# Performance work log

Hardware: AMD Instinct MI355X
Metric: run time of the kernel (lower is better)

Reference implementation:

```python
import jax, jax.numpy as jnp
import numpy as np

B, T, C, H = 8, 1024, 768, 12
M = 8  # extra rows in feats left as zeros (n = M + B*T)
N = M + B * T


def setup_inputs() -> dict:
    key = jax.random.key(0)
    k1, k2, k3, k4, k5 = jax.random.split(key, 5)
    feats = jax.random.normal(k1, (N, C), dtype=jnp.float32)
    amask = jax.random.randint(k2, (B, T), 0, 2).astype(bool)
    Wqkv = jax.random.normal(k3, (3 * C, C), dtype=jnp.float32) * 0.02
    Wp = jax.random.normal(k4, (C, C), dtype=jnp.float32) * 0.02
    bp = jax.random.normal(k5, (C,), dtype=jnp.float32) * 0.001
    return {"feats": feats, "amask": amask, "Wqkv": Wqkv, "Wp": Wp, "bp": bp}


def reference(feats, amask, Wqkv, Wp, bp):
    b, t = amask.shape
    n, c = feats.shape
    m = n - b * t          # rows of feats not touched by attention (stay zero)
    h = H
    d = c // h
    scale = d ** -0.5
    mf = amask.reshape(-1)                      # [b*t] bool
    x = feats[m:]                               # [b*t, c]

    # MaskedLinear(qkv): gather->GEMM->scatter == dense GEMM zeroed at masked-out rows
    qkv = jnp.where(mf[:, None], x @ Wqkv.T, jnp.zeros((), x.dtype))  # [b*t, 3c]
    qkv = qkv.reshape(b, t, 3, h, d).transpose(2, 0, 3, 1, 4)          # [3,b,h,t,d]
    q, k, v = qkv[0], qkv[1], qkv[2]

    # dense SDPA (no attn mask, matching F.scaled_dot_product_attention default)
    att = jax.nn.softmax(jnp.einsum('bhqd,bhkd->bhqk', q, k) * scale, axis=-1)
    o = jnp.einsum('bhqk,bhkd->bhqd', att, v)                          # [b,h,t,d]
    o = o.transpose(0, 2, 1, 3).reshape(b * t, c)                      # [b*t, c]

    # MaskedLinear(proj) with bias; masked-out rows are zero (not bias)
    o = jnp.where(mf[:, None], o @ Wp.T + bp, jnp.zeros((), o.dtype))

    # scatter back into a zero tensor of feats' shape (first m rows zero)
    return jnp.concatenate([jnp.zeros((m, c), feats.dtype), o], axis=0)
```

## Files before the change

### kernel.cpp

```cpp
#include <hip/hip_runtime.h>
#include <hip/hip_bf16.h>


#define BB 8
#define TT 1024
#define CC 768
#define HH 12
#define DD 64
#define MM 8
#define NTOK (BB*TT)
#define NX (NTOK*CC)
#define NWQ (3*CC*CC)
#define NWP (CC*CC)
#define QSCALE 0.18033688011112042f

typedef short bf16x8 __attribute__((ext_vector_type(8)));
typedef float f32x4  __attribute__((ext_vector_type(4)));
typedef float f32x16 __attribute__((ext_vector_type(16)));

__device__ __forceinline__ void gld16(const void* g, void* l) {
  __builtin_amdgcn_global_load_lds(
      (const __attribute__((address_space(1))) void*)g,
      (__attribute__((address_space(3))) void*)l, 16, 0, 0);
}

__device__ __forceinline__ short bf_rne(float f) {
  unsigned u = __float_as_uint(f);
  return (short)((u + 0x7FFFu + ((u >> 16) & 1u)) >> 16);
}
__device__ __forceinline__ short bf_split(float f, short& lo) {
  unsigned u = __float_as_uint(f);
  unsigned hb = (u + 0x7FFFu + ((u >> 16) & 1u)) >> 16;
  float r = f - __uint_as_float(hb << 16);
  lo = bf_rne(r);
  return (short)hb;
}

__global__ __launch_bounds__(256) void split_inputs(
    const float* __restrict__ x, const float* __restrict__ wq,
    const float* __restrict__ wp,
    short* __restrict__ xh, short* __restrict__ wqh,
    short* __restrict__ wph, short* __restrict__ wpl) {
  const int G0 = NX/4, G1 = G0 + NWQ/4, G2 = G1 + NWP/4;
  int i = blockIdx.x * 256 + threadIdx.x;
  if (i >= G2) return;
  if (i < G1) {
    const float* src = (i < G0) ? x : wq;
    short* dh = (i < G0) ? xh : wqh;
    int li = (i < G0) ? i : i - G0;
    float4 v = *(const float4*)(src + (size_t)li * 4);
    short4 h;
    h.x = bf_rne(v.x); h.y = bf_rne(v.y); h.z = bf_rne(v.z); h.w = bf_rne(v.w);
    *(short4*)(dh + (size_t)li * 4) = h;
  } else {
    int li = i - G1;
    float4 v = *(const float4*)(wp + (size_t)li * 4);
    short4 h, l;
    h.x = bf_split(v.x, l.x);
    h.y = bf_split(v.y, l.y);
    h.z = bf_split(v.z, l.z);
    h.w = bf_split(v.w, l.w);
    *(short4*)(wph + (size_t)li * 4) = h;
    *(short4*)(wpl + (size_t)li * 4) = l;
  }
}

template<bool TRIPLE>
__device__ __forceinline__ void gemm_core_768(
    const short* __restrict__ ah_g, const short* __restrict__ al_g,
    const short* __restrict__ bh_g, const short* __restrict__ bl_g,
    int m0, int n0, f32x16 (&acc)[2][2],
    int& wm_o, int& wn_o) {
  __shared__ __align__(16) short Ah[128*32], Bh[128*32];
  __shared__ __align__(16) short Al[TRIPLE ? 128*32 : 16];
  __shared__ __align__(16) short Bl[TRIPLE ? 128*32 : 16];
  const int tid = threadIdx.x;
  const int w = tid >> 6, ln = tid & 63;
  const int wm = (w >> 1) * 64, wn = (w & 1) * 64;
  const int sr = ln >> 2, sc = (ln & 3) * 8;
  const int l31 = ln & 31, lhi = ln >> 5;
  const int c0 = 2*w, c1 = 2*w + 1;
  const short* gAh0 = ah_g + (size_t)(m0 + c0*16 + sr)*CC + sc;
  const short* gAh1 = ah_g + (size_t)(m0 + c1*16 + sr)*CC + sc;
  const short* gBh0 = bh_g + (size_t)(n0 + c0*16 + sr)*CC + sc;
  const short* gBh1 = bh_g + (size_t)(n0 + c1*16 + sr)*CC + sc;
  const short* gAl0 = TRIPLE ? al_g + (size_t)(m0 + c0*16 + sr)*CC + sc : nullptr;
  const short* gAl1 = TRIPLE ? al_g + (size_t)(m0 + c1*16 + sr)*CC + sc : nullptr;
  const short* gBl0 = TRIPLE ? bl_g + (size_t)(n0 + c0*16 + sr)*CC + sc : nullptr;
  const short* gBl1 = TRIPLE ? bl_g + (size_t)(n0 + c1*16 + sr)*CC + sc : nullptr;
  #pragma unroll
  for (int i = 0; i < 2; i++)
    #pragma unroll
    for (int j = 0; j < 2; j++)
      #pragma unroll
      for (int r = 0; r < 16; r++) acc[i][j][r] = 0.f;

  for (int it = 0; it < 24; ++it) {
    const int ko = it * 32;
    gld16(gAh0 + ko, &Ah[c0*512]);
    gld16(gAh1 + ko, &Ah[c1*512]);
    gld16(gBh0 + ko, &Bh[c0*512]);
    gld16(gBh1 + ko, &Bh[c1*512]);
    if constexpr (TRIPLE) {
      gld16(gAl0 + ko, &Al[c0*512]);
      gld16(gAl1 + ko, &Al[c1*512]);
      gld16(gBl0 + ko, &Bl[c0*512]);
      gld16(gBl1 + ko, &Bl[c1*512]);
    }
    __syncthreads();
    bf16x8 a_h[2][2], b_h[2][2];
    #pragma unroll
    for (int t = 0; t < 2; ++t)
      #pragma unroll
      for (int kc = 0; kc < 2; ++kc) {
        a_h[t][kc] = *(const bf16x8*)&Ah[(wm + t*32 + l31)*32 + kc*16 + lhi*8];
        b_h[t][kc] = *(const bf16x8*)&Bh[(wn + t*32 + l31)*32 + kc*16 + lhi*8];
      }
    if constexpr (TRIPLE) {
      bf16x8 a_l[2][2], b_l[2][2];
      #pragma unroll
      for (int t = 0; t < 2; ++t)
        #pragma unroll
        for (int kc = 0; kc < 2; ++kc) {
          a_l[t][kc] = *(const bf16x8*)&Al[(wm + t*32 + l31)*32 + kc*16 + lhi*8];
          b_l[t][kc] = *(const bf16x8*)&Bl[(wn + t*32 + l31)*32 + kc*16 + lhi*8];
        }
      #pragma unroll
      for (int mt = 0; mt < 2; ++mt)
        #pragma unroll
        for (int nt = 0; nt < 2; ++nt)
          #pragma unroll
          for (int kc = 0; kc < 2; ++kc) {
            acc[mt][nt] = __builtin_amdgcn_mfma_f32_32x32x16_bf16(
                a_h[mt][kc], b_h[nt][kc], acc[mt][nt], 0, 0, 0);
            acc[mt][nt] = __builtin_amdgcn_mfma_f32_32x32x16_bf16(
                a_h[mt][kc], b_l[nt][kc], acc[mt][nt], 0, 0, 0);
            acc[mt][nt] = __builtin_amdgcn_mfma_f32_32x32x16_bf16(
                a_l[mt][kc], b_h[nt][kc], acc[mt][nt], 0, 0, 0);
          }
    } else {
      #pragma unroll
      for (int mt = 0; mt < 2; ++mt)
        #pragma unroll
        for (int nt = 0; nt < 2; ++nt)
          #pragma unroll
          for (int kc = 0; kc < 2; ++kc)
            acc[mt][nt] = __builtin_amdgcn_mfma_f32_32x32x16_bf16(
                a_h[mt][kc], b_h[nt][kc], acc[mt][nt], 0, 0, 0);
    }
    __syncthreads();
  }
  wm_o = wm; wn_o = wn;
}

__global__ __launch_bounds__(256) void qkv_mfma(
    const short* __restrict__ ah_g, const short* __restrict__ bh_g,
    const int* __restrict__ mask,
    short* __restrict__ qb, short* __restrict__ kb, short* __restrict__ vb) {
  const int m0 = blockIdx.y * 128, n0 = blockIdx.x * 128;
  f32x16 acc[2][2];
  int wm, wn;
  gemm_core_768<false>(ah_g, nullptr, bh_g, nullptr, m0, n0, acc, wm, wn);
  const int ln = threadIdx.x & 63;
  const int l31 = ln & 31, lhi = ln >> 5;
  const int s = n0 / CC;
  short* dst = (s == 0) ? qb : ((s == 1) ? kb : vb);
  const float qs = (s == 0) ? QSCALE : 1.f;
  const int nb = n0 % CC;
  #pragma unroll
  for (int mt = 0; mt < 2; ++mt) {
    #pragma unroll
    for (int reg = 0; reg < 16; ++reg) {
      int row = m0 + wm + mt*32 + 4*lhi + (reg & 3) + 8*(reg >> 2);
      int mk = mask[row];
      int b = row >> 10, t = row & 1023;
      size_t rb = ((size_t)b * HH) * TT;
      #pragma unroll
      for (int nt = 0; nt < 2; ++nt) {
        int gnb = nb + wn + nt*32 + l31;
        int h = gnb >> 6, d = gnb & 63;
        float v = mk ? acc[mt][nt][reg] * qs : 0.f;
        dst[((rb + (size_t)h * TT) + t) * DD + d] = bf_rne(v);
      }
    }
  }
}

__global__ __launch_bounds__(256) void proj_mfma(
    const short* __restrict__ ah_g, const short* __restrict__ al_g,
    const short* __restrict__ bh_g, const short* __restrict__ bl_g,
    const int* __restrict__ mask, const float* __restrict__ bp,
    float* __restrict__ out) {
  const int m0 = blockIdx.y * 128, n0 = blockIdx.x * 128;
  f32x16 acc[2][2];
  int wm, wn;
  gemm_core_768<true>(ah_g, al_g, bh_g, bl_g, m0, n0, acc, wm, wn);
  const int ln = threadIdx.x & 63;
  const int l31 = ln & 31, lhi = ln >> 5;
  #pragma unroll
  for (int mt = 0; mt < 2; ++mt) {
    #pragma unroll
    for (int reg = 0; reg < 16; ++reg) {
      int row = m0 + wm + mt*32 + 4*lhi + (reg & 3) + 8*(reg >> 2);
      int mk = mask[row];
      float* orow = out + (size_t)(MM + row) * CC;
      #pragma unroll
      for (int nt = 0; nt < 2; ++nt) {
        int gn = n0 + wn + nt*32 + l31;
        orow[gn] = mk ? acc[mt][nt][reg] + bp[gn] : 0.f;
      }
    }
  }
}

__global__ __launch_bounds__(256) void attn_mfma(
    const short* __restrict__ qb, const short* __restrict__ kb,
    const short* __restrict__ vb, const int* __restrict__ mask,
    short* __restrict__ obh, short* __restrict__ obl) {
  __shared__ __align__(16) short Ks[64][72];
  __shared__ __align__(16) short Vt[64][72];
  __shared__ __align__(16) short Ps[4][32][72];
  const int tid = threadIdx.x, w = tid >> 6, ln = tid & 63;
  const int fl = ln & 15, fq = ln >> 4;
  const int bh = blockIdx.x >> 3;
  const int q0 = (blockIdx.x & 7) * 128;
  const int b = bh / HH, h = bh % HH;
  const size_t base = (size_t)bh * TT * DD;

  bf16x8 qf[2][2];
  #pragma unroll
  for (int mt = 0; mt < 2; ++mt)
    #pragma unroll
    for (int kc = 0; kc < 2; ++kc)
      qf[mt][kc] = *(const bf16x8*)&qb[base +
          (size_t)(q0 + w*32 + mt*16 + fl) * DD + kc*32 + fq*8];

  f32x4 oa[2][4];
  float lsum[2][4];
  {
    f32x4 z = {0.f, 0.f, 0.f, 0.f};
    #pragma unroll
    for (int mt = 0; mt < 2; ++mt) {
      #pragma unroll
      for (int nt = 0; nt < 4; ++nt) oa[mt][nt] = z;
      #pragma unroll
      for (int r = 0; r < 4; ++r) lsum[mt][r] = 0.f;
    }
  }

  const int skey = tid >> 2, sch = (tid & 3) * 2;
  const int vkey = tid & 63, vd0 = (tid >> 6) * 16;

  for (int kt = 0; kt < 16; ++kt) {
    __syncthreads();
    {
      const short* kg = &kb[base + (size_t)(kt*64 + skey) * DD + sch*8];
      bf16x8 k0 = *(const bf16x8*)kg;
      bf16x8 k1 = *(const bf16x8*)(kg + 8);
      *(bf16x8*)&Ks[skey][sch*8] = k0;
      *(bf16x8*)&Ks[skey][sch*8 + 8] = k1;
      const short* vg = &vb[base + (size_t)(kt*64 + vkey) * DD + vd0];
      bf16x8 v0 = *(const bf16x8*)vg;
      bf16x8 v1 = *(const bf16x8*)(vg + 8);
      #pragma unroll
      for (int j = 0; j < 8; ++j) {
        Vt[vd0 + j][vkey] = v0[j];
        Vt[vd0 + 8 + j][vkey] = v1[j];
      }
    }
    __syncthreads();

    bf16x8 kf[4][2], vf[4][2];
    #pragma unroll
    for (int nt = 0; nt < 4; ++nt)
      #pragma unroll
      for (int kc = 0; kc < 2; ++kc) {
        kf[nt][kc] = *(const bf16x8*)&Ks[nt*16 + fl][kc*32 + fq*8];
        vf[nt][kc] = *(const bf16x8*)&Vt[nt*16 + fl][kc*32 + fq*8];
      }

    f32x4 s[2][4];
    {
      f32x4 z = {0.f, 0.f, 0.f, 0.f};
      #pragma unroll
      for (int mt = 0; mt < 2; ++mt)
        #pragma unroll
        for (int nt = 0; nt < 4; ++nt) s[mt][nt] = z;
    }
    #pragma unroll
    for (int mt = 0; mt < 2; ++mt)
      #pragma unroll
      for (int nt = 0; nt < 4; ++nt) {
        s[mt][nt] = __builtin_amdgcn_mfma_f32_16x16x32_bf16(
            qf[mt][0], kf[nt][0], s[mt][nt], 0, 0, 0);
        s[mt][nt] = __builtin_amdgcn_mfma_f32_16x16x32_bf16(
            qf[mt][1], kf[nt][1], s[mt][nt], 0, 0, 0);
      }

    #pragma unroll
    for (int mt = 0; mt < 2; ++mt)
      #pragma unroll
      for (int nt = 0; nt < 4; ++nt)
        #pragma unroll
        for (int r = 0; r < 4; ++r) {
          float p = __builtin_amdgcn_exp2f(s[mt][nt][r]);
          unsigned pu = __float_as_uint(p);
          lsum[mt][r] += __uint_as_float(pu & 0xFFFF0000u);
          Ps[w][mt*16 + fq*4 + r][nt*16 + fl] = (short)(pu >> 16);
        }

    bf16x8 pf[2][2];
    #pragma unroll
    for (int mt = 0; mt < 2; ++mt)
      #pragma unroll
      for (int kc = 0; kc < 2; ++kc)
        pf[mt][kc] = *(const bf16x8*)&Ps[w][mt*16 + fl][kc*32 + fq*8];

    #pragma unroll
    for (int mt = 0; mt < 2; ++mt)
      #pragma unroll
      for (int nt = 0; nt < 4; ++nt) {
        oa[mt][nt] = __builtin_amdgcn_mfma_f32_16x16x32_bf16(
            pf[mt][0], vf[nt][0], oa[mt][nt], 0, 0, 0);
        oa[mt][nt] = __builtin_amdgcn_mfma_f32_16x16x32_bf16(
            pf[mt][1], vf[nt][1], oa[mt][nt], 0, 0, 0);
      }
  }

  #pragma unroll
  for (int mt = 0; mt < 2; ++mt)
    #pragma unroll
    for (int r = 0; r < 4; ++r) {
      float v = lsum[mt][r];
      v += __shfl_xor(v, 1);
      v += __shfl_xor(v, 2);
      v += __shfl_xor(v, 4);
      v += __shfl_xor(v, 8);
      lsum[mt][r] = v;
    }

  #pragma unroll
  for (int mt = 0; mt < 2; ++mt)
    #pragma unroll
    for (int r = 0; r < 4; ++r) {
      int tok = b * TT + q0 + w*32 + mt*16 + fq*4 + r;
      int mk = mask[tok];
      float inv = 1.f / lsum[mt][r];
      size_t ro = (size_t)tok * CC + h * DD;
      #pragma unroll
      for (int nt = 0; nt < 4; ++nt) {
        float v = mk ? oa[mt][nt][r] * inv : 0.f;
        short lo, hi = bf_split(v, lo);
        obh[ro + nt*16 + fl] = hi;
        obl[ro + nt*16 + fl] = lo;
      }
    }
}

__global__ void zero_head(float* __restrict__ out) {
  int i = blockIdx.x * 256 + threadIdx.x;
  if (i < MM * CC) out[i] = 0.f;
}

extern "C" void kernel_launch(void* const* d_in, const int* in_sizes, int n_in,
                              void* d_out, int out_size, void* d_ws, size_t ws_size,
                              hipStream_t stream) {
  const float* feats = (const float*)d_in[0];
  const int*   mask  = (const int*)d_in[1];
  const float* Wqkv  = (const float*)d_in[2];
  const float* Wp    = (const float*)d_in[3];
  const float* bp    = (const float*)d_in[4];
  float* out = (float*)d_out;

  short* qb   = (short*)d_ws;
  short* kb   = qb + NX;
  short* vb   = kb + NX;
  short* S_hi = vb + NX;
  short* S_lo = S_hi + NX;
  short* wqh  = S_lo + NX;
  short* wph  = wqh + NWQ;
  short* wpl  = wph + NWP;

  const int G2 = (NX + NWQ + NWP) / 4;
  split_inputs<<<dim3((G2 + 255)/256), dim3(256), 0, stream>>>(
      feats + (size_t)MM * CC, Wqkv, Wp, S_hi, wqh, wph, wpl);
  qkv_mfma<<<dim3(3*CC/128, NTOK/128), dim3(256), 0, stream>>>(
      S_hi, wqh, mask, qb, kb, vb);
  attn_mfma<<<dim3(BB*HH*(TT/128)), dim3(256), 0, stream>>>(
      qb, kb, vb, mask, S_hi, S_lo);
  proj_mfma<<<dim3(CC/128, NTOK/128), dim3(256), 0, stream>>>(
      S_hi, S_lo, wph, wpl, mask, bp, out);
  zero_head<<<dim3((MM*CC + 255)/256), dim3(256), 0, stream>>>(out);
}
```

Baseline: 257.0 us.

## Write V pre-transposed from QKV GEMM and read K/V directly from global in attention

The QKV GEMM epilogue for the V slice now stages the tile in shared memory and writes V in a [b,h,d,t] transposed layout. The attention kernel drops its shared-memory K/V staging, the transpose and the block barriers. It uses single-wave blocks of 32 queries that load K and V MFMA fragments straight from global memory. The aim is to remove LDS transpose and sync overhead, at the cost of each wave re-reading K/V from global/L2 with no sharing across waves.

New measurement: 296.5 us. 1.15x slower.

```diff
diff --git a/kernel.cpp b/kernel.cpp
--- a/kernel.cpp
+++ b/kernel.cpp
@@ -69,11 +69,9 @@
 __device__ __forceinline__ void gemm_core_768(
     const short* __restrict__ ah_g, const short* __restrict__ al_g,
     const short* __restrict__ bh_g, const short* __restrict__ bl_g,
+    short* Ah, short* Al, short* Bh, short* Bl,
     int m0, int n0, f32x16 (&acc)[2][2],
     int& wm_o, int& wn_o) {
-  __shared__ __align__(16) short Ah[128*32], Bh[128*32];
-  __shared__ __align__(16) short Al[TRIPLE ? 128*32 : 16];
-  __shared__ __align__(16) short Bl[TRIPLE ? 128*32 : 16];
   const int tid = threadIdx.x;
   const int w = tid >> 6, ln = tid & 63;
   const int wm = (w >> 1) * 64, wn = (w & 1) * 64;
@@ -156,33 +154,60 @@
 __global__ __launch_bounds__(256) void qkv_mfma(
     const short* __restrict__ ah_g, const short* __restrict__ bh_g,
     const int* __restrict__ mask,
-    short* __restrict__ qb, short* __restrict__ kb, short* __restrict__ vb) {
+    short* __restrict__ qb, short* __restrict__ kb, short* __restrict__ vbt) {
+  __shared__ __align__(16) short SMEM[128*132];
   const int m0 = blockIdx.y * 128, n0 = blockIdx.x * 128;
   f32x16 acc[2][2];
   int wm, wn;
-  gemm_core_768<false>(ah_g, nullptr, bh_g, nullptr, m0, n0, acc, wm, wn);
-  const int ln = threadIdx.x & 63;
+  gemm_core_768<false>(ah_g, nullptr, bh_g, nullptr,
+                       SMEM, SMEM, SMEM + 4096, SMEM + 4096, m0, n0, acc, wm, wn);
+  const int tid = threadIdx.x, ln = tid & 63;
   const int l31 = ln & 31, lhi = ln >> 5;
   const int s = n0 / CC;
-  short* dst = (s == 0) ? qb : ((s == 1) ? kb : vb);
-  const float qs = (s == 0) ? QSCALE : 1.f;
   const int nb = n0 % CC;
-  #pragma unroll
-  for (int mt = 0; mt < 2; ++mt) {
-    #pragma unroll
-    for (int reg = 0; reg < 16; ++reg) {
-      int row = m0 + wm + mt*32 + 4*lhi + (reg & 3) + 8*(reg >> 2);
-      int mk = mask[row];
-      int b = row >> 10, t = row & 1023;
-      size_t rb = ((size_t)b * HH) * TT;
-      #pragma unroll
-      for (int nt = 0; nt < 2; ++nt) {
-        int gnb = nb + wn + nt*32 + l31;
-        int h = gnb >> 6, d = gnb & 63;
-        float v = mk ? acc[mt][nt][reg] * qs : 0.f;
-        dst[((rb + (size_t)h * TT) + t) * DD + d] = bf_rne(v);
+  if (s < 2) {
+    short* dst = (s == 0) ? qb : kb;
+    const float qs = (s == 0) ? QSCALE : 1.f;
+    #pragma unroll
+    for (int mt = 0; mt < 2; ++mt) {
+      #pragma unroll
+      for (int reg = 0; reg < 16; ++reg) {
+        int row = m0 + wm + mt*32 + 4*lhi + (reg & 3) + 8*(reg >> 2);
+        int mk = mask[row];
+        int b = row >> 10, t = row & 1023;
+        size_t rb = ((size_t)b * HH) * TT;
+        #pragma unroll
+        for (int nt = 0; nt < 2; ++nt) {
+          int gnb = nb + wn + nt*32 + l31;
+          int h = gnb >> 6, d = gnb & 63;
+          float v = mk ? acc[mt][nt][reg] * qs : 0.f;
+          dst[((rb + (size_t)h * TT) + t) * DD + d] = bf_rne(v);
+        }
       }
     }
+  } else {
+    #pragma unroll
+    for (int mt = 0; mt < 2; ++mt) {
+      #pragma unroll
+      for (int reg = 0; reg < 16; ++reg) {
+        int rl = wm + mt*32 + 4*lhi + (reg & 3) + 8*(reg >> 2);
+        int mk = mask[m0 + rl];
+        #pragma unroll
+        for (int nt = 0; nt < 2; ++nt) {
+          int cl = wn + nt*32 + l31;
+          SMEM[cl*132 + rl] = bf_rne(mk ? acc[mt][nt][reg] : 0.f);
+        }
+      }
+    }
+    __syncthreads();
+    const int c = tid >> 1, half = tid & 1;
+    const int h = (nb + c) >> 6, d = (nb + c) & 63;
+    const int b = m0 >> 10, t0 = (m0 & 1023) + half*64;
+    short* dstp = vbt + (((size_t)(b*HH + h)*DD + d)*TT) + t0;
+    const short* srcp = &SMEM[c*132 + half*64];
+    #pragma unroll
+    for (int g = 0; g < 8; ++g)
+      *(bf16x8*)(dstp + g*8) = *(const bf16x8*)(srcp + g*8);
   }
 }
 
@@ -191,10 +216,12 @@
     const short* __restrict__ bh_g, const short* __restrict__ bl_g,
     const int* __restrict__ mask, const float* __restrict__ bp,
     float* __restrict__ out) {
+  __shared__ __align__(16) short Ah[128*32], Al[128*32];
+  __shared__ __align__(16) short Bh[128*32], Bl[128*32];
   const int m0 = blockIdx.y * 128, n0 = blockIdx.x * 128;
   f32x16 acc[2][2];
   int wm, wn;
-  gemm_core_768<true>(ah_g, al_g, bh_g, bl_g, m0, n0, acc, wm, wn);
+  gemm_core_768<true>(ah_g, al_g, bh_g, bl_g, Ah, Al, Bh, Bl, m0, n0, acc, wm, wn);
   const int ln = threadIdx.x & 63;
   const int l31 = ln & 31, lhi = ln >> 5;
   #pragma unroll
@@ -213,27 +240,26 @@
   }
 }
 
-__global__ __launch_bounds__(256) void attn_mfma(
+__global__ __launch_bounds__(64) void attn_mfma(
     const short* __restrict__ qb, const short* __restrict__ kb,
-    const short* __restrict__ vb, const int* __restrict__ mask,
+    const short* __restrict__ vbt, const int* __restrict__ mask,
     short* __restrict__ obh, short* __restrict__ obl) {
-  __shared__ __align__(16) short Ks[64][72];
-  __shared__ __align__(16) short Vt[64][72];
-  __shared__ __align__(16) short Ps[4][32][72];
-  const int tid = threadIdx.x, w = tid >> 6, ln = tid & 63;
+  __shared__ __align__(16) short Ps[32][72];
+  const int ln = threadIdx.x;
   const int fl = ln & 15, fq = ln >> 4;
-  const int bh = blockIdx.x >> 3;
-  const int q0 = (blockIdx.x & 7) * 128;
+  const int bh = blockIdx.x >> 5;
+  const int q0 = (blockIdx.x & 31) * 32;
   const int b = bh / HH, h = bh % HH;
-  const size_t base = (size_t)bh * TT * DD;
+  const size_t baseK = (size_t)bh * TT * DD;
+  const size_t baseV = (size_t)bh * DD * TT;
 
   bf16x8 qf[2][2];
   #pragma unroll
   for (int mt = 0; mt < 2; ++mt)
     #pragma unroll
     for (int kc = 0; kc < 2; ++kc)
-      qf[mt][kc] = *(const bf16x8*)&qb[base +
-          (size_t)(q0 + w*32 + mt*16 + fl) * DD + kc*32 + fq*8];
+      qf[mt][kc] = *(const bf16x8*)&qb[baseK +
+          (size_t)(q0 + mt*16 + fl) * DD + kc*32 + fq*8];
 
   f32x4 oa[2][4];
   float lsum[2][4];
@@ -248,37 +274,7 @@
     }
   }
 
-  const int skey = tid >> 2, sch = (tid & 3) * 2;
-  const int vkey = tid & 63, vd0 = (tid >> 6) * 16;
-
   for (int kt = 0; kt < 16; ++kt) {
-    __syncthreads();
-    {
-      const short* kg = &kb[base + (size_t)(kt*64 + skey) * DD + sch*8];
-      bf16x8 k0 = *(const bf16x8*)kg;
-      bf16x8 k1 = *(const bf16x8*)(kg + 8);
-      *(bf16x8*)&Ks[skey][sch*8] = k0;
-      *(bf16x8*)&Ks[skey][sch*8 + 8] = k1;
-      const short* vg = &vb[base + (size_t)(kt*64 + vkey) * DD + vd0];
-      bf16x8 v0 = *(const bf16x8*)vg;
-      bf16x8 v1 = *(const bf16x8*)(vg + 8);
-      #pragma unroll
-      for (int j = 0; j < 8; ++j) {
-        Vt[vd0 + j][vkey] = v0[j];
-        Vt[vd0 + 8 + j][vkey] = v1[j];
-      }
-    }
-    __syncthreads();
-
-    bf16x8 kf[4][2], vf[4][2];
-    #pragma unroll
-    for (int nt = 0; nt < 4; ++nt)
-      #pragma unroll
-      for (int kc = 0; kc < 2; ++kc) {
-        kf[nt][kc] = *(const bf16x8*)&Ks[nt*16 + fl][kc*32 + fq*8];
-        vf[nt][kc] = *(const bf16x8*)&Vt[nt*16 + fl][kc*32 + fq*8];
-      }
-
     f32x4 s[2][4];
     {
       f32x4 z = {0.f, 0.f, 0.f, 0.f};
@@ -288,14 +284,19 @@
         for (int nt = 0; nt < 4; ++nt) s[mt][nt] = z;
     }
     #pragma unroll
-    for (int mt = 0; mt < 2; ++mt)
-      #pragma unroll
-      for (int nt = 0; nt < 4; ++nt) {
-        s[mt][nt] = __builtin_amdgcn_mfma_f32_16x16x32_bf16(
-            qf[mt][0], kf[nt][0], s[mt][nt], 0, 0, 0);
-        s[mt][nt] = __builtin_amdgcn_mfma_f32_16x16x32_bf16(
-            qf[mt][1], kf[nt][1], s[mt][nt], 0, 0, 0);
-      }
+    for (int kc = 0; kc < 2; ++kc) {
+      bf16x8 kf[4];
+      #pragma unroll
+      for (int nt = 0; nt < 4; ++nt)
+        kf[nt] = *(const bf16x8*)&kb[baseK +
+            (size_t)(kt*64 + nt*16 + fl) * DD + kc*32 + fq*8];
+      #pragma unroll
+      for (int mt = 0; mt < 2; ++mt)
+        #pragma unroll
+        for (int nt = 0; nt < 4; ++nt)
+          s[mt][nt] = __builtin_amdgcn_mfma_f32_16x16x32_bf16(
+              qf[mt][kc], kf[nt], s[mt][nt], 0, 0, 0);
+    }
 
     #pragma unroll
     for (int mt = 0; mt < 2; ++mt)
@@ -306,7 +307,7 @@
           float p = __builtin_amdgcn_exp2f(s[mt][nt][r]);
           unsigned pu = __float_as_uint(p);
           lsum[mt][r] += __uint_as_float(pu & 0xFFFF0000u);
-          Ps[w][mt*16 + fq*4 + r][nt*16 + fl] = (short)(pu >> 16);
+          Ps[mt*16 + fq*4 + r][nt*16 + fl] = (short)(pu >> 16);
         }
 
     bf16x8 pf[2][2];
@@ -314,17 +315,22 @@
     for (int mt = 0; mt < 2; ++mt)
       #pragma unroll
       for (int kc = 0; kc < 2; ++kc)
-        pf[mt][kc] = *(const bf16x8*)&Ps[w][mt*16 + fl][kc*32 + fq*8];
-
-    #pragma unroll
-    for (int mt = 0; mt < 2; ++mt)
-      #pragma unroll
-      for (int nt = 0; nt < 4; ++nt) {
-        oa[mt][nt] = __builtin_amdgcn_mfma_f32_16x16x32_bf16(
-            pf[mt][0], vf[nt][0], oa[mt][nt], 0, 0, 0);
-        oa[mt][nt] = __builtin_amdgcn_mfma_f32_16x16x32_bf16(
-            pf[mt][1], vf[nt][1], oa[mt][nt], 0, 0, 0);
-      }
+        pf[mt][kc] = *(const bf16x8*)&Ps[mt*16 + fl][kc*32 + fq*8];
+
+    #pragma unroll
+    for (int kc = 0; kc < 2; ++kc) {
+      bf16x8 vf[4];
+      #pragma unroll
+      for (int nt = 0; nt < 4; ++nt)
+        vf[nt] = *(const bf16x8*)&vbt[baseV +
+            (size_t)(nt*16 + fl) * TT + kt*64 + kc*32 + fq*8];
+      #pragma unroll
+      for (int mt = 0; mt < 2; ++mt)
+        #pragma unroll
+        for (int nt = 0; nt < 4; ++nt)
+          oa[mt][nt] = __builtin_amdgcn_mfma_f32_16x16x32_bf16(
+              pf[mt][kc], vf[nt], oa[mt][nt], 0, 0, 0);
+    }
   }
 
   #pragma unroll
@@ -343,7 +349,7 @@
   for (int mt = 0; mt < 2; ++mt)
     #pragma unroll
     for (int r = 0; r < 4; ++r) {
-      int tok = b * TT + q0 + w*32 + mt*16 + fq*4 + r;
+      int tok = b * TT + q0 + mt*16 + fq*4 + r;
       int mk = mask[tok];
       float inv = 1.f / lsum[mt][r];
       size_t ro = (size_t)tok * CC + h * DD;
@@ -374,8 +380,8 @@
 
   short* qb   = (short*)d_ws;
   short* kb   = qb + NX;
-  short* vb   = kb + NX;
-  short* S_hi = vb + NX;
+  short* vbt  = kb + NX;
+  short* S_hi = vbt + NX;
   short* S_lo = S_hi + NX;
   short* wqh  = S_lo + NX;
   short* wph  = wqh + NWQ;
@@ -385,9 +391,9 @@
   split_inputs<<<dim3((G2 + 255)/256), dim3(256), 0, stream>>>(
       feats + (size_t)MM * CC, Wqkv, Wp, S_hi, wqh, wph, wpl);
   qkv_mfma<<<dim3(3*CC/128, NTOK/128), dim3(256), 0, stream>>>(
-      S_hi, wqh, mask, qb, kb, vb);
-  attn_mfma<<<dim3(BB*HH*(TT/128)), dim3(256), 0, stream>>>(
-      qb, kb, vb, mask, S_hi, S_lo);
+      S_hi, wqh, mask, qb, kb, vbt);
+  attn_mfma<<<dim3(BB*HH*(TT/32)), dim3(64), 0, stream>>>(
+      qb, kb, vbt, mask, S_hi, S_lo);
   proj_mfma<<<dim3(CC/128, NTOK/128), dim3(256), 0, stream>>>(
       S_hi, S_lo, wph, wpl, mask, bp, out);
   zero_head<<<dim3((MM*CC + 255)/256), dim3(256), 0, stream>>>(out);
```
